# Kernel tuning notes

Measured on AMD Instinct MI355X. Metric: run time of the kernel, lower is better.

The kernel has to match this reference:

```python
import jax, jax.numpy as jnp
import numpy as np

EPS = 1e-05
B, M, N, P = 32, 1024, 1024, 256


def _xavier(key, shape):
    fan_in, fan_out = shape[0], shape[1]
    limit = np.sqrt(6.0 / (fan_in + fan_out))
    return jax.random.uniform(key, shape, jnp.float32, -limit, limit)


def setup_inputs() -> dict:
    key = jax.random.key(0)
    ks = jax.random.split(key, 6)
    return {
        "x": jax.random.normal(ks[0], (B, M, N), jnp.float32),
        "original_xj_y": _xavier(ks[1], (N, P)),
        "original_xi_y": _xavier(ks[2], (M, P)),
        "permuted_xj_y": _xavier(ks[3], (M, P)),
        "permuted_xi_y": _xavier(ks[4], (N, P)),
        "gamma_o_sum": jnp.ones((P,), jnp.float32),
        "gamma_o": jnp.ones((P, P), jnp.float32),
        "gamma_p_sum": jnp.ones((P,), jnp.float32),
        "gamma_p": jnp.ones((P, P), jnp.float32),
        "gamma": jnp.ones((P, P), jnp.float32),
        "beta_o_sum": jnp.zeros((P,), jnp.float32),
        "beta_o": jnp.zeros((P, P), jnp.float32),
        "beta_p_sum": jnp.zeros((P,), jnp.float32),
        "beta_p": jnp.zeros((P, P), jnp.float32),
        "beta": jnp.zeros((P, P), jnp.float32),
    }


def _normalize(x, axes, gamma, beta):
    mean = jnp.mean(x, axis=axes, keepdims=True)
    std = jnp.sqrt(jnp.var(x, axis=axes, keepdims=True, ddof=1))  # torch std is unbiased
    return gamma * ((x - mean) / (std + EPS)) + beta


def reference(x, original_xj_y, original_xi_y, permuted_xj_y, permuted_xi_y,
              gamma_o_sum, gamma_o, gamma_p_sum, gamma_p, gamma,
              beta_o_sum, beta_o, beta_p_sum, beta_p, beta):
    permuted = jnp.swapaxes(x, -1, -2)  # [B, N, M]

    # original path
    oyy = x @ original_xj_y                      # [B, M, P]
    o_sum = _normalize(oyy.sum(axis=-2), (-1,), gamma_o_sum, beta_o_sum) + 1.0  # [B, P]
    oyy = jnp.swapaxes(oyy, -1, -2) @ original_xi_y  # [B, P, P]
    oyy = jnp.swapaxes(oyy, -1, -2)
    oyy = _normalize(oyy, (-2, -1), gamma_o, beta_o)

    # permuted path
    pyy = permuted @ permuted_xj_y               # [B, N, P]
    p_sum = _normalize(pyy.sum(axis=-2), (-1,), gamma_p_sum, beta_p_sum) + 1.0  # [B, P]
    pyy = jnp.swapaxes(pyy, -1, -2) @ permuted_xi_y  # [B, P, P]
    pyy = jnp.swapaxes(pyy, -1, -2)
    pyy = _normalize(pyy, (-2, -1), gamma_p, beta_p)

    relations = jnp.einsum('ij,ik->ijk', o_sum, p_sum)  # [B, P, P]
    projected = (oyy * relations) @ (pyy * relations)   # [B, P, P]
    projected = _normalize(projected, (-2, -1), gamma, beta)
    return (projected, relations)
```

## Files before the change

### kernel.cpp

```cpp
#include <hip/hip_runtime.h>
#include <hip/hip_bf16.h>

#define PP 256
#define BB 32
#define MM 1024
#define NN 1024

constexpr float EPSF = 1e-5f;

typedef __attribute__((ext_vector_type(8))) short short8v;
typedef __attribute__((ext_vector_type(4))) short short4v;
typedef __attribute__((ext_vector_type(4))) float f32x4;

__device__ inline float bf2f(short s) {
  union { unsigned u; float f; } cv;
  cv.u = ((unsigned)(unsigned short)s) << 16;
  return cv.f;
}
__device__ inline short f2bf(float f) {
  union { float f; unsigned u; } cv; cv.f = f;
  unsigned u = cv.u;
  unsigned r = (u + 0x7fffu + ((u >> 16) & 1u)) >> 16;
  return (short)r;
}

__device__ inline void gload16(const void* g, void* l) {
  __builtin_amdgcn_global_load_lds(
      (const __attribute__((address_space(1))) unsigned*)g,
      (__attribute__((address_space(3))) unsigned*)l, 16, 0, 0);
}

__global__ __launch_bounds__(256)
void wconv4(const float* __restrict__ s0, const float* __restrict__ s1,
            const float* __restrict__ s2, const float* __restrict__ s3,
            short* __restrict__ d0, short* __restrict__ d1,
            short* __restrict__ d2, short* __restrict__ d3)
{
  const float* src = (blockIdx.z == 0) ? s0 : (blockIdx.z == 1) ? s1
                    : (blockIdx.z == 2) ? s2 : s3;
  short* dst = (blockIdx.z == 0) ? d0 : (blockIdx.z == 1) ? d1
              : (blockIdx.z == 2) ? d2 : d3;
  __shared__ float tile[64][65];
  const int c0 = blockIdx.x * 64, r0 = blockIdx.y * 64;
  const int tid = threadIdx.x;
#pragma unroll
  for (int i = 0; i < 16; ++i) {
    int idx = i * 256 + tid;
    int r = idx >> 6, c = idx & 63;
    tile[r][c] = src[(long)(r0 + r) * 256 + (c0 + c)];
  }
  __syncthreads();
#pragma unroll
  for (int i = 0; i < 16; ++i) {
    int idx = i * 256 + tid;
    int rr = idx >> 6, cc = idx & 63;
    dst[(long)(c0 + rr) * 1024 + (r0 + cc)] = f2bf(tile[cc][rr]);
  }
}

__global__ __launch_bounds__(256)
void tr2_f32(const float* __restrict__ s0, const float* __restrict__ s1,
             float* __restrict__ d0, float* __restrict__ d1)
{
  const float* src = blockIdx.z ? s1 : s0;
  float* dst = blockIdx.z ? d1 : d0;
  __shared__ float tile[64][65];
  const int c0 = blockIdx.x * 64, r0 = blockIdx.y * 64;
  const int tid = threadIdx.x;
#pragma unroll
  for (int i = 0; i < 16; ++i) {
    int idx = i * 256 + tid;
    int r = idx >> 6, c = idx & 63;
    tile[r][c] = src[(long)(r0 + r) * 256 + (c0 + c)];
  }
  __syncthreads();
#pragma unroll
  for (int i = 0; i < 16; ++i) {
    int idx = i * 256 + tid;
    int rr = idx >> 6, cc = idx & 63;
    dst[(long)(c0 + rr) * 256 + (r0 + cc)] = tile[cc][rr];
  }
}

__global__ __launch_bounds__(256)
void gemm_xcat(const float* __restrict__ x, const short* __restrict__ wcat,
               short* __restrict__ oyyT, short* __restrict__ UT,
               float* __restrict__ rowsum)
{
  __shared__ short As[2][4096];
  __shared__ short Bs[3][4096];

  const int hwid = blockIdx.x;
  const int work = (hwid & 7) * 128 + (hwid >> 3);
  const int nblk = work & 3;
  const int mblk = (work >> 2) & 7;
  const int b    = work >> 5;

  const float* Ab = x + (long)b * MM * NN;
  const int m0 = mblk * 128;
  const int n0 = nblk * 128;

  const int tid = threadIdx.x;
  const int l = tid & 63, w = tid >> 6;
  const int wr = w >> 1, wc = w & 1;
  const int lk = l >> 4, lr = l & 15;
  const int sm = tid >> 2, skc = tid & 3;

  const float* aptr0 = Ab + (long)(m0 + sm) * NN + skc * 8;
  const float* aptr1 = aptr0 + 64 * NN;
  const int sA0 = ((skc * 128 + sm) * 8) ^ (skc << 4);
  const int sA1 = ((skc * 128 + 64 + sm) * 8) ^ (skc << 4);

  const int bn0 = tid & 127, bkc0 = tid >> 7;
  const int bn1 = bn0, bkc1 = bkc0 + 2;
  const short* bptrA = wcat + (long)(n0 + bn0) * NN + bkc0 * 8;
  const short* bptrB = wcat + (long)(n0 + bn1) * NN + bkc1 * 8;
  const int sBA = tid * 8, sBB = (tid + 256) * 8;

  f32x4 acc[4][4];
#pragma unroll
  for (int fm = 0; fm < 4; ++fm)
#pragma unroll
    for (int fn = 0; fn < 4; ++fn)
      acc[fm][fn] = (f32x4){0.f, 0.f, 0.f, 0.f};

  float rs0 = 0.f, rs1 = 0.f;
  const bool doRs = (nblk == 0);
  float4 a00, a01, a10, a11;

#define XC_LOAD_A(k0_) do { \
    a00 = *reinterpret_cast<const float4*>(aptr0 + (k0_)); \
    a01 = *reinterpret_cast<const float4*>(aptr0 + (k0_) + 4); \
    a10 = *reinterpret_cast<const float4*>(aptr1 + (k0_)); \
    a11 = *reinterpret_cast<const float4*>(aptr1 + (k0_) + 4); \
  } while (0)

#define XC_STAGE_B(buf_, k0_) do { \
    gload16(bptrA + (k0_), &Bs[buf_][sBA]); \
    gload16(bptrB + (k0_), &Bs[buf_][sBB]); \
  } while (0)

#define XC_STAGE_A(buf_) do { \
    if (doRs) { \
      rs0 += a00.x + a00.y + a00.z + a00.w + a01.x + a01.y + a01.z + a01.w; \
      rs1 += a10.x + a10.y + a10.z + a10.w + a11.x + a11.y + a11.z + a11.w; \
    } \
    short8v pk0, pk1; \
    pk0[0] = f2bf(a00.x); pk0[1] = f2bf(a00.y); pk0[2] = f2bf(a00.z); pk0[3] = f2bf(a00.w); \
    pk0[4] = f2bf(a01.x); pk0[5] = f2bf(a01.y); pk0[6] = f2bf(a01.z); pk0[7] = f2bf(a01.w); \
    pk1[0] = f2bf(a10.x); pk1[1] = f2bf(a10.y); pk1[2] = f2bf(a10.z); pk1[3] = f2bf(a10.w); \
    pk1[4] = f2bf(a11.x); pk1[5] = f2bf(a11.y); pk1[6] = f2bf(a11.z); pk1[7] = f2bf(a11.w); \
    *reinterpret_cast<short8v*>(&As[buf_][sA0]) = pk0; \
    *reinterpret_cast<short8v*>(&As[buf_][sA1]) = pk1; \
  } while (0)

  XC_LOAD_A(0);
  XC_STAGE_B(0, 0);
  XC_STAGE_B(1, 32);
  XC_STAGE_A(0);
  asm volatile("s_waitcnt vmcnt(2) lgkmcnt(0)" ::: "memory");
  __builtin_amdgcn_s_barrier();
  __builtin_amdgcn_sched_barrier(0);

  int curB = 0, nxtB = 2;
  int curA = 0;
  for (int kt = 0; kt < 32; ++kt) {
    if (kt < 31) XC_LOAD_A((kt + 1) * 32);
    if (kt < 30) XC_STAGE_B(nxtB, (kt + 2) * 32);

    short8v af[4], bf[4];
#pragma unroll
    for (int fm = 0; fm < 4; ++fm) {
      const int row = wr * 64 + fm * 16 + lr;
      af[fm] = *reinterpret_cast<const short8v*>(
          &As[curA][((lk * 128 + row) * 8) ^ (lk << 4)]);
    }
#pragma unroll
    for (int fn = 0; fn < 4; ++fn)
      bf[fn] = *reinterpret_cast<const short8v*>(
          &Bs[curB][(lk * 128 + wc * 64 + fn * 16 + lr) * 8]);
#pragma unroll
    for (int fm = 0; fm < 4; ++fm)
#pragma unroll
      for (int fn = 0; fn < 4; ++fn)
        acc[fm][fn] = __builtin_amdgcn_mfma_f32_16x16x32_bf16(
            af[fm], bf[fn], acc[fm][fn], 0, 0, 0);

    if (kt < 31) XC_STAGE_A(curA ^ 1);
    asm volatile("s_waitcnt vmcnt(2) lgkmcnt(0)" ::: "memory");
    __builtin_amdgcn_s_barrier();
    __builtin_amdgcn_sched_barrier(0);
    curA ^= 1;
    curB = (curB == 2) ? 0 : curB + 1;
    nxtB = (nxtB == 2) ? 0 : nxtB + 1;
  }

  if (doRs) {
    rs0 += __shfl_xor(rs0, 1); rs0 += __shfl_xor(rs0, 2);
    rs1 += __shfl_xor(rs1, 1); rs1 += __shfl_xor(rs1, 2);
    if (skc == 0) {
      rowsum[(long)b * MM + m0 + sm] = rs0;
      rowsum[(long)b * MM + m0 + 64 + sm] = rs1;
    }
  }

  short* Cb = ((n0 < 256) ? oyyT : UT) + (long)b * PP * MM;
  const int nb = n0 & 255;
#pragma unroll
  for (int fm = 0; fm < 4; ++fm)
#pragma unroll
    for (int fn = 0; fn < 4; ++fn) {
      const int c = nb + wc * 64 + fn * 16 + lr;
      const int rb = m0 + wr * 64 + fm * 16 + lk * 4;
      short4v pk;
#pragma unroll
      for (int j = 0; j < 4; ++j) pk[j] = f2bf(acc[fm][fn][j]);
      *reinterpret_cast<short4v*>(&Cb[(long)c * MM + rb]) = pk;
    }
}

__global__ __launch_bounds__(256)
void colsum_bf16(const short* __restrict__ srcT, float* __restrict__ raw)
{
  const int b = blockIdx.y;
  const int w = threadIdx.x >> 6, l = threadIdx.x & 63;
  const int p = blockIdx.x * 4 + w;
  const short* row = srcT + ((long)b * 256 + p) * 1024;
  short8v v1 = *(const short8v*)&row[l * 8];
  short8v v2 = *(const short8v*)&row[(64 + l) * 8];
  float s = 0.f;
#pragma unroll
  for (int j = 0; j < 8; ++j) s += bf2f(v1[j]) + bf2f(v2[j]);
#pragma unroll
  for (int off = 32; off; off >>= 1) s += __shfl_down(s, off);
  if (l == 0) raw[(long)b * 256 + p] = s;
}

__global__ __launch_bounds__(256)
void psum_dot(const short* __restrict__ wp1T, const float* __restrict__ rowsum,
              float* __restrict__ rawP)
{
  __shared__ float rsm[1024];
  const int b = blockIdx.x;
  for (int i = threadIdx.x; i < 1024; i += 256) rsm[i] = rowsum[(long)b * 1024 + i];
  __syncthreads();
  const int p = threadIdx.x;
  const short* wrow = wp1T + (long)p * 1024;
  float s = 0.f;
  for (int k = 0; k < 1024; k += 8) {
    short8v v = *(const short8v*)&wrow[k];
#pragma unroll
    for (int j = 0; j < 8; ++j) s = fmaf(bf2f(v[j]), rsm[k + j], s);
  }
  rawP[(long)b * 256 + p] = s;
}

__device__ inline void block_reduce2(float& v1, float& v2, float* red)
{
#pragma unroll
  for (int off = 32; off > 0; off >>= 1) {
    v1 += __shfl_down(v1, off);
    v2 += __shfl_down(v2, off);
  }
  const int lane = threadIdx.x & 63, wid = threadIdx.x >> 6;
  if (lane == 0) { red[wid * 2] = v1; red[wid * 2 + 1] = v2; }
  __syncthreads();
  v1 = red[0] + red[2] + red[4] + red[6];
  v2 = red[1] + red[3] + red[5] + red[7];
}

__global__ __launch_bounds__(256)
void norm_sum2(const float* __restrict__ raw2,
               const float* __restrict__ g_os, const float* __restrict__ b_os,
               const float* __restrict__ g_ps, const float* __restrict__ b_ps,
               float* __restrict__ o_sum, float* __restrict__ p_sum)
{
  const int bb = blockIdx.x;
  const bool isP = bb >= 32;
  const int b = bb & 31;
  const float* raw = raw2 + (isP ? 8192 : 0);
  const float* gamma = isP ? g_ps : g_os;
  const float* beta = isP ? b_ps : b_os;
  float* outp = isP ? p_sum : o_sum;
  const int p = threadIdx.x;
  float s = raw[(long)b * 256 + p];
  __shared__ float red[8];
  float v1 = s, v2 = s * s;
  block_reduce2(v1, v2, red);
  const float mean = v1 / 256.0f;
  float var = fmaxf((v2 - v1 * mean) / 255.0f, 0.f);
  const float inv = 1.0f / (sqrtf(var) + EPSF);
  outp[(long)b * 256 + p] = gamma[p] * (s - mean) * inv + beta[p] + 1.0f;
}

__global__ __launch_bounds__(256)
void gemm_dual(const short* __restrict__ oyyT, const short* __restrict__ wo2T,
               const short* __restrict__ UT, const short* __restrict__ wp1T,
               float* __restrict__ t2T, float* __restrict__ p2)
{
  constexpr int BM = 64, BN = 64;
  __shared__ short As[2][4 * BM * 8];
  __shared__ short Bs[2][4 * BN * 8];

  const int z = blockIdx.z;
  const short* Ab; const short* Bb; float* Cb;
  if (z < 32) { Ab = oyyT + (long)z * PP * MM; Bb = wo2T; Cb = t2T + ((long)z << 16); }
  else { Ab = UT + (long)(z - 32) * PP * MM; Bb = wp1T; Cb = p2 + ((long)(z - 32) << 16); }

  const int m0 = blockIdx.x * BM, n0 = blockIdx.y * BN;
  const int tid = threadIdx.x;
  const int l = tid & 63, w = tid >> 6;
  const int wr = w >> 1, wc = w & 1;
  const int lk = l >> 4, lr = l & 15;
  const int kc = tid >> 6, mloc = tid & 63;
  const short* aP = Ab + (long)(m0 + mloc) * MM + kc * 8;
  const short* bP = Bb + (long)(n0 + mloc) * MM + kc * 8;

  f32x4 acc[2][2];
#pragma unroll
  for (int fm = 0; fm < 2; ++fm)
#pragma unroll
    for (int fn = 0; fn < 2; ++fn)
      acc[fm][fn] = (f32x4){0.f, 0.f, 0.f, 0.f};

  gload16(aP, &As[0][tid * 8]);
  gload16(bP, &Bs[0][tid * 8]);
  __syncthreads();

  for (int kt = 0; kt < 32; ++kt) {
    const int cur = kt & 1, nxt = cur ^ 1;
    if (kt < 31) {
      gload16(aP + (kt + 1) * 32, &As[nxt][tid * 8]);
      gload16(bP + (kt + 1) * 32, &Bs[nxt][tid * 8]);
    }
    short8v af[2], bf[2];
#pragma unroll
    for (int fm = 0; fm < 2; ++fm)
      af[fm] = *(const short8v*)&As[cur][(lk * BM + wr * 32 + fm * 16 + lr) * 8];
#pragma unroll
    for (int fn = 0; fn < 2; ++fn)
      bf[fn] = *(const short8v*)&Bs[cur][(lk * BN + wc * 32 + fn * 16 + lr) * 8];
#pragma unroll
    for (int fm = 0; fm < 2; ++fm)
#pragma unroll
      for (int fn = 0; fn < 2; ++fn)
        acc[fm][fn] = __builtin_amdgcn_mfma_f32_16x16x32_bf16(
            af[fm], bf[fn], acc[fm][fn], 0, 0, 0);
    __syncthreads();
  }

#pragma unroll
  for (int fm = 0; fm < 2; ++fm)
#pragma unroll
    for (int fn = 0; fn < 2; ++fn) {
      const int c = n0 + wc * 32 + fn * 16 + lr;
      const int rb = m0 + wr * 32 + fm * 16 + lk * 4;
      *(f32x4*)&Cb[(long)c * PP + rb] = acc[fm][fn];
    }
}

__global__ __launch_bounds__(256)
void gemm_pp(const short* __restrict__ A, const short* __restrict__ BT,
             float* __restrict__ C)
{
  constexpr int BM = 64, BN = 64;
  __shared__ short As[2][4 * BM * 8];
  __shared__ short Bs[2][4 * BN * 8];
  const int b = blockIdx.z;
  const short* Ab = A + ((long)b << 16);
  const short* Bb = BT + ((long)b << 16);
  float* Cb = C + ((long)b << 16);
  const int m0 = blockIdx.x * BM, n0 = blockIdx.y * BN;
  const int tid = threadIdx.x;
  const int l = tid & 63, w = tid >> 6;
  const int wr = w >> 1, wc = w & 1;
  const int lk = l >> 4, lr = l & 15;
  const int kc = tid >> 6, mloc = tid & 63;
  const short* aP = Ab + (long)(m0 + mloc) * PP + kc * 8;
  const short* bP = Bb + (long)(n0 + mloc) * PP + kc * 8;

  f32x4 acc[2][2];
#pragma unroll
  for (int fm = 0; fm < 2; ++fm)
#pragma unroll
    for (int fn = 0; fn < 2; ++fn)
      acc[fm][fn] = (f32x4){0.f, 0.f, 0.f, 0.f};

  gload16(aP, &As[0][tid * 8]);
  gload16(bP, &Bs[0][tid * 8]);
  __syncthreads();

  for (int kt = 0; kt < 8; ++kt) {
    const int cur = kt & 1, nxt = cur ^ 1;
    if (kt < 7) {
      gload16(aP + (kt + 1) * 32, &As[nxt][tid * 8]);
      gload16(bP + (kt + 1) * 32, &Bs[nxt][tid * 8]);
    }
    short8v af[2], bf[2];
#pragma unroll
    for (int fm = 0; fm < 2; ++fm)
      af[fm] = *(const short8v*)&As[cur][(lk * BM + wr * 32 + fm * 16 + lr) * 8];
#pragma unroll
    for (int fn = 0; fn < 2; ++fn)
      bf[fn] = *(const short8v*)&Bs[cur][(lk * BN + wc * 32 + fn * 16 + lr) * 8];
#pragma unroll
    for (int fm = 0; fm < 2; ++fm)
#pragma unroll
      for (int fn = 0; fn < 2; ++fn)
        acc[fm][fn] = __builtin_amdgcn_mfma_f32_16x16x32_bf16(
            af[fm], bf[fn], acc[fm][fn], 0, 0, 0);
    __syncthreads();
  }

#pragma unroll
  for (int fm = 0; fm < 2; ++fm)
#pragma unroll
    for (int fn = 0; fn < 2; ++fn) {
      const int c = n0 + wc * 32 + fn * 16 + lr;
      const int rb = m0 + wr * 32 + fm * 16 + lk * 4;
#pragma unroll
      for (int j = 0; j < 4; ++j)
        Cb[(long)(rb + j) * PP + c] = acc[fm][fn][j];
    }
}

__global__ __launch_bounds__(256)
void stats_dual(const float* __restrict__ t2T, const float* __restrict__ p2,
                float* __restrict__ part)
{
  const int y = blockIdx.y, chunk = blockIdx.x;
  const float* s = (y < 32 ? t2T + ((long)y << 16)
                           : p2 + ((long)(y - 32) << 16)) + (long)chunk * 8192;
  float v1 = 0.f, v2 = 0.f;
  for (int i = threadIdx.x; i < 2048; i += 256) {
    float4 xv = *reinterpret_cast<const float4*>(&s[i * 4]);
    v1 += xv.x + xv.y + xv.z + xv.w;
    v2 = fmaf(xv.x, xv.x, fmaf(xv.y, xv.y, fmaf(xv.z, xv.z, fmaf(xv.w, xv.w, v2))));
  }
  __shared__ float red[8];
  block_reduce2(v1, v2, red);
  if (threadIdx.x == 0) {
    part[(y * 8 + chunk) * 2] = v1;
    part[(y * 8 + chunk) * 2 + 1] = v2;
  }
}

__global__ void stats_fin2(const float* __restrict__ part,
                           float* __restrict__ stO, float* __restrict__ stP)
{
  const int t = threadIdx.x;
  float v1 = 0.f, v2 = 0.f;
#pragma unroll
  for (int c = 0; c < 8; ++c) {
    v1 += part[(t * 8 + c) * 2];
    v2 += part[(t * 8 + c) * 2 + 1];
  }
  const float mean = v1 / 65536.0f;
  const float var = fmaxf((v2 - v1 * mean) / 65535.0f, 0.f);
  float* st = (t < 32) ? stO : stP;
  st[(t & 31) * 2] = mean;
  st[(t & 31) * 2 + 1] = 1.0f / (sqrtf(var) + EPSF);
}

__global__ __launch_bounds__(256)
void stats_part(const float* __restrict__ src, float* __restrict__ part)
{
  const int b = blockIdx.y, chunk = blockIdx.x;
  const float* s = src + ((long)b << 16) + (long)chunk * 8192;
  float v1 = 0.f, v2 = 0.f;
  for (int i = threadIdx.x; i < 2048; i += 256) {
    float4 xv = *reinterpret_cast<const float4*>(&s[i * 4]);
    v1 += xv.x + xv.y + xv.z + xv.w;
    v2 = fmaf(xv.x, xv.x, fmaf(xv.y, xv.y, fmaf(xv.z, xv.z, fmaf(xv.w, xv.w, v2))));
  }
  __shared__ float red[8];
  block_reduce2(v1, v2, red);
  if (threadIdx.x == 0) {
    part[(b * 8 + chunk) * 2] = v1;
    part[(b * 8 + chunk) * 2 + 1] = v2;
  }
}

__global__ void stats_fin(const float* __restrict__ part, float* __restrict__ st)
{
  const int b = threadIdx.x;
  if (b < 32) {
    float v1 = 0.f, v2 = 0.f;
#pragma unroll
    for (int c = 0; c < 8; ++c) {
      v1 += part[(b * 8 + c) * 2];
      v2 += part[(b * 8 + c) * 2 + 1];
    }
    const float mean = v1 / 65536.0f;
    const float var = fmaxf((v2 - v1 * mean) / 65535.0f, 0.f);
    st[b * 2] = mean;
    st[b * 2 + 1] = 1.0f / (sqrtf(var) + EPSF);
  }
}

__global__ __launch_bounds__(256)
void prep2(const float* __restrict__ t2T, const float* __restrict__ p2,
           const float* __restrict__ o_sum, const float* __restrict__ p_sum,
           const float* __restrict__ gamma_o, const float* __restrict__ beta_o,
           const float* __restrict__ gTp, const float* __restrict__ bTp,
           const float* __restrict__ stO, const float* __restrict__ stP,
           short* __restrict__ Ap, short* __restrict__ BpT,
           float* __restrict__ out)
{
  const long idx = (long)blockIdx.x * 256 + threadIdx.x;
  const int b = (int)(idx >> 16);
  const int rc = (int)(idx & 65535);
  const int r = rc >> 8, c = rc & 255;
  const float mO = stO[b * 2], iO = stO[b * 2 + 1];
  const float mP = stP[b * 2], iP = stP[b * 2 + 1];
  const float relA = o_sum[(b << 8) + r] * p_sum[(b << 8) + c];
  const float on = gamma_o[rc] * (t2T[idx] - mO) * iO + beta_o[rc];
  Ap[idx] = f2bf(on * relA);
  const float pn = gTp[rc] * (p2[idx] - mP) * iP + bTp[rc];
  BpT[idx] = f2bf(pn * o_sum[(b << 8) + c] * p_sum[(b << 8) + r]);
  out[(long)BB * 65536 + idx] = relA;
}

__global__ __launch_bounds__(256)
void final_half(const float* __restrict__ proj, const float* __restrict__ stF,
                const float* __restrict__ gamma, const float* __restrict__ beta,
                float* __restrict__ out)
{
  const long idx = (long)blockIdx.x * 256 + threadIdx.x;
  const int b = (int)(idx >> 16);
  const int ij = (int)(idx & 65535);
  out[idx] = gamma[ij] * (proj[idx] - stF[b * 2]) * stF[b * 2 + 1] + beta[ij];
}

extern "C" void kernel_launch(void* const* d_in, const int* in_sizes, int n_in,
                              void* d_out, int out_size, void* d_ws, size_t ws_size,
                              hipStream_t stream)
{
  const float* x    = (const float*)d_in[0];
  const float* Wo1  = (const float*)d_in[1];
  const float* Wo2  = (const float*)d_in[2];
  const float* Wp1  = (const float*)d_in[3];
  const float* Wp2  = (const float*)d_in[4];
  const float* g_os = (const float*)d_in[5];
  const float* g_o  = (const float*)d_in[6];
  const float* g_ps = (const float*)d_in[7];
  const float* g_p  = (const float*)d_in[8];
  const float* g    = (const float*)d_in[9];
  const float* b_os = (const float*)d_in[10];
  const float* b_o  = (const float*)d_in[11];
  const float* b_ps = (const float*)d_in[12];
  const float* b_p  = (const float*)d_in[13];
  const float* b_   = (const float*)d_in[14];
  float* out = (float*)d_out;

  short* wcat = (short*)d_ws;
  short* wo2T = wcat + 524288;
  short* wp1T = wo2T + 262144;
  short* oyyT = wp1T + 262144;
  short* UT   = oyyT + 8388608;
  float* gTp  = (float*)(UT + 8388608);
  float* bTp  = gTp + 65536;
  float* rowsumX = bTp + 65536;
  float* t2T  = rowsumX + 32768;
  float* p2   = t2T + 2097152;
  float* proj = p2 + 2097152;
  short* Ap   = (short*)(proj + 2097152);
  short* BpT  = Ap + 2097152;
  float* raw2 = (float*)(BpT + 2097152);
  float* o_sum = raw2 + 16384;
  float* p_sum = o_sum + 8192;
  float* part  = p_sum + 8192;
  float* partF = part + 1024;
  float* stO   = partF + 512;
  float* stP   = stO + 64;
  float* stF   = stP + 64;

  wconv4<<<dim3(4, 16, 4), 256, 0, stream>>>(Wo1, Wo2, Wp1, Wp2,
                                             wcat, wo2T, wp1T, wcat + 262144);
  tr2_f32<<<dim3(4, 4, 2), 256, 0, stream>>>(g_p, b_p, gTp, bTp);

  gemm_xcat<<<dim3(1024, 1, 1), 256, 0, stream>>>(x, wcat, oyyT, UT, rowsumX);

  colsum_bf16<<<dim3(64, 32), 256, 0, stream>>>(oyyT, raw2);
  psum_dot<<<32, 256, 0, stream>>>(wp1T, rowsumX, raw2 + 8192);
  norm_sum2<<<64, 256, 0, stream>>>(raw2, g_os, b_os, g_ps, b_ps, o_sum, p_sum);

  gemm_dual<<<dim3(4, 4, 64), 256, 0, stream>>>(oyyT, wo2T, UT, wp1T, t2T, p2);

  stats_dual<<<dim3(8, 64), 256, 0, stream>>>(t2T, p2, part);
  stats_fin2<<<1, 64, 0, stream>>>(part, stO, stP);

  prep2<<<8192, 256, 0, stream>>>(t2T, p2, o_sum, p_sum, g_o, b_o, gTp, bTp,
                                  stO, stP, Ap, BpT, out);

  gemm_pp<<<dim3(4, 4, 32), 256, 0, stream>>>(Ap, BpT, proj);

  stats_part<<<dim3(8, 32), 256, 0, stream>>>(proj, partF);
  stats_fin<<<1, 64, 0, stream>>>(partF, stF);

  final_half<<<8192, 256, 0, stream>>>(proj, stF, g, b_, out);
}
```

Baseline: 191.8 us.

## Halve N tile of x-GEMM to 64 and use hardware bf16 pack conversion

```diff
diff --git a/kernel.cpp b/kernel.cpp
--- a/kernel.cpp
+++ b/kernel.cpp
@@ -22,6 +22,21 @@
   unsigned u = cv.u;
   unsigned r = (u + 0x7fffu + ((u >> 16) & 1u)) >> 16;
   return (short)r;
+}
+
+__device__ inline short8v cvt8(float4 lo, float4 hi) {
+  union { int i[4]; short8v s; } u;
+  asm("v_cvt_pk_bf16_f32 %0, %1, %2" : "=v"(u.i[0]) : "v"(lo.x), "v"(lo.y));
+  asm("v_cvt_pk_bf16_f32 %0, %1, %2" : "=v"(u.i[1]) : "v"(lo.z), "v"(lo.w));
+  asm("v_cvt_pk_bf16_f32 %0, %1, %2" : "=v"(u.i[2]) : "v"(hi.x), "v"(hi.y));
+  asm("v_cvt_pk_bf16_f32 %0, %1, %2" : "=v"(u.i[3]) : "v"(hi.z), "v"(hi.w));
+  return u.s;
+}
+__device__ inline short4v cvt4(f32x4 v) {
+  union { int i[2]; short4v s; } u;
+  asm("v_cvt_pk_bf16_f32 %0, %1, %2" : "=v"(u.i[0]) : "v"(v[0]), "v"(v[1]));
+  asm("v_cvt_pk_bf16_f32 %0, %1, %2" : "=v"(u.i[1]) : "v"(v[2]), "v"(v[3]));
+  return u.s;
 }
 
 __device__ inline void gload16(const void* g, void* l) {
@@ -88,17 +103,17 @@
                float* __restrict__ rowsum)
 {
   __shared__ short As[2][4096];
-  __shared__ short Bs[3][4096];
+  __shared__ short Bs[3][2048];
 
   const int hwid = blockIdx.x;
-  const int work = (hwid & 7) * 128 + (hwid >> 3);
-  const int nblk = work & 3;
-  const int mblk = (work >> 2) & 7;
-  const int b    = work >> 5;
+  const int work = (hwid & 7) * 256 + (hwid >> 3);
+  const int nblk = work & 7;
+  const int mblk = (work >> 3) & 7;
+  const int b    = work >> 6;
 
   const float* Ab = x + (long)b * MM * NN;
   const int m0 = mblk * 128;
-  const int n0 = nblk * 128;
+  const int n0 = nblk * 64;
 
   const int tid = threadIdx.x;
   const int l = tid & 63, w = tid >> 6;
@@ -108,20 +123,16 @@
 
   const float* aptr0 = Ab + (long)(m0 + sm) * NN + skc * 8;
   const float* aptr1 = aptr0 + 64 * NN;
+  const short* bptr = wcat + (long)(n0 + (tid & 63)) * NN + (tid >> 6) * 8;
+  const int sB = tid * 8;
   const int sA0 = ((skc * 128 + sm) * 8) ^ (skc << 4);
   const int sA1 = ((skc * 128 + 64 + sm) * 8) ^ (skc << 4);
 
-  const int bn0 = tid & 127, bkc0 = tid >> 7;
-  const int bn1 = bn0, bkc1 = bkc0 + 2;
-  const short* bptrA = wcat + (long)(n0 + bn0) * NN + bkc0 * 8;
-  const short* bptrB = wcat + (long)(n0 + bn1) * NN + bkc1 * 8;
-  const int sBA = tid * 8, sBB = (tid + 256) * 8;
-
-  f32x4 acc[4][4];
+  f32x4 acc[4][2];
 #pragma unroll
   for (int fm = 0; fm < 4; ++fm)
 #pragma unroll
-    for (int fn = 0; fn < 4; ++fn)
+    for (int fn = 0; fn < 2; ++fn)
       acc[fm][fn] = (f32x4){0.f, 0.f, 0.f, 0.f};
 
   float rs0 = 0.f, rs1 = 0.f;
@@ -135,30 +146,22 @@
     a11 = *reinterpret_cast<const float4*>(aptr1 + (k0_) + 4); \
   } while (0)
 
-#define XC_STAGE_B(buf_, k0_) do { \
-    gload16(bptrA + (k0_), &Bs[buf_][sBA]); \
-    gload16(bptrB + (k0_), &Bs[buf_][sBB]); \
-  } while (0)
+#define XC_STAGE_B(buf_, k0_) gload16(bptr + (k0_), &Bs[buf_][sB])
 
 #define XC_STAGE_A(buf_) do { \
     if (doRs) { \
       rs0 += a00.x + a00.y + a00.z + a00.w + a01.x + a01.y + a01.z + a01.w; \
       rs1 += a10.x + a10.y + a10.z + a10.w + a11.x + a11.y + a11.z + a11.w; \
     } \
-    short8v pk0, pk1; \
-    pk0[0] = f2bf(a00.x); pk0[1] = f2bf(a00.y); pk0[2] = f2bf(a00.z); pk0[3] = f2bf(a00.w); \
-    pk0[4] = f2bf(a01.x); pk0[5] = f2bf(a01.y); pk0[6] = f2bf(a01.z); pk0[7] = f2bf(a01.w); \
-    pk1[0] = f2bf(a10.x); pk1[1] = f2bf(a10.y); pk1[2] = f2bf(a10.z); pk1[3] = f2bf(a10.w); \
-    pk1[4] = f2bf(a11.x); pk1[5] = f2bf(a11.y); pk1[6] = f2bf(a11.z); pk1[7] = f2bf(a11.w); \
-    *reinterpret_cast<short8v*>(&As[buf_][sA0]) = pk0; \
-    *reinterpret_cast<short8v*>(&As[buf_][sA1]) = pk1; \
+    *reinterpret_cast<short8v*>(&As[buf_][sA0]) = cvt8(a00, a01); \
+    *reinterpret_cast<short8v*>(&As[buf_][sA1]) = cvt8(a10, a11); \
   } while (0)
 
   XC_LOAD_A(0);
   XC_STAGE_B(0, 0);
   XC_STAGE_B(1, 32);
   XC_STAGE_A(0);
-  asm volatile("s_waitcnt vmcnt(2) lgkmcnt(0)" ::: "memory");
+  asm volatile("s_waitcnt vmcnt(1) lgkmcnt(0)" ::: "memory");
   __builtin_amdgcn_s_barrier();
   __builtin_amdgcn_sched_barrier(0);
 
@@ -168,7 +171,7 @@
     if (kt < 31) XC_LOAD_A((kt + 1) * 32);
     if (kt < 30) XC_STAGE_B(nxtB, (kt + 2) * 32);
 
-    short8v af[4], bf[4];
+    short8v af[4], bf[2];
 #pragma unroll
     for (int fm = 0; fm < 4; ++fm) {
       const int row = wr * 64 + fm * 16 + lr;
@@ -176,18 +179,18 @@
           &As[curA][((lk * 128 + row) * 8) ^ (lk << 4)]);
     }
 #pragma unroll
-    for (int fn = 0; fn < 4; ++fn)
+    for (int fn = 0; fn < 2; ++fn)
       bf[fn] = *reinterpret_cast<const short8v*>(
-          &Bs[curB][(lk * 128 + wc * 64 + fn * 16 + lr) * 8]);
+          &Bs[curB][(lk * 64 + wc * 32 + fn * 16 + lr) * 8]);
 #pragma unroll
     for (int fm = 0; fm < 4; ++fm)
 #pragma unroll
-      for (int fn = 0; fn < 4; ++fn)
+      for (int fn = 0; fn < 2; ++fn)
         acc[fm][fn] = __builtin_amdgcn_mfma_f32_16x16x32_bf16(
             af[fm], bf[fn], acc[fm][fn], 0, 0, 0);
 
     if (kt < 31) XC_STAGE_A(curA ^ 1);
-    asm volatile("s_waitcnt vmcnt(2) lgkmcnt(0)" ::: "memory");
+    asm volatile("s_waitcnt vmcnt(1) lgkmcnt(0)" ::: "memory");
     __builtin_amdgcn_s_barrier();
     __builtin_amdgcn_sched_barrier(0);
     curA ^= 1;
@@ -198,7 +201,7 @@
   if (doRs) {
     rs0 += __shfl_xor(rs0, 1); rs0 += __shfl_xor(rs0, 2);
     rs1 += __shfl_xor(rs1, 1); rs1 += __shfl_xor(rs1, 2);
-    if (skc == 0) {
+    if ((tid & 3) == 0) {
       rowsum[(long)b * MM + m0 + sm] = rs0;
       rowsum[(long)b * MM + m0 + 64 + sm] = rs1;
     }
@@ -209,13 +212,10 @@
 #pragma unroll
   for (int fm = 0; fm < 4; ++fm)
 #pragma unroll
-    for (int fn = 0; fn < 4; ++fn) {
-      const int c = nb + wc * 64 + fn * 16 + lr;
+    for (int fn = 0; fn < 2; ++fn) {
+      const int c = nb + wc * 32 + fn * 16 + lr;
       const int rb = m0 + wr * 64 + fm * 16 + lk * 4;
-      short4v pk;
-#pragma unroll
-      for (int j = 0; j < 4; ++j) pk[j] = f2bf(acc[fm][fn][j]);
-      *reinterpret_cast<short4v*>(&Cb[(long)c * MM + rb]) = pk;
+      *reinterpret_cast<short4v*>(&Cb[(long)c * MM + rb]) = cvt4(acc[fm][fn]);
     }
 }
 
@@ -579,7 +579,7 @@
                                              wcat, wo2T, wp1T, wcat + 262144);
   tr2_f32<<<dim3(4, 4, 2), 256, 0, stream>>>(g_p, b_p, gTp, bTp);
 
-  gemm_xcat<<<dim3(1024, 1, 1), 256, 0, stream>>>(x, wcat, oyyT, UT, rowsumX);
+  gemm_xcat<<<dim3(2048, 1, 1), 256, 0, stream>>>(x, wcat, oyyT, UT, rowsumX);
 
   colsum_bf16<<<dim3(64, 32), 256, 0, stream>>>(oyyT, raw2);
   psum_dot<<<32, 256, 0, stream>>>(wp1T, rowsumX, raw2 + 8192);
```

Result: faster. 186.4 us (-2.8%).
